# Kernel tuning notes

Hardware: AMD Instinct MI355X
Metric: run time of the kernel (lower is better)

Reference implementation:

```python
import jax, jax.numpy as jnp
import numpy as np

INPUT_SIZE = 84 * 84 * 4  # 28224
FEATURE_SIZE = 1500
BATCH = 256

def setup_inputs() -> dict:
    key = jax.random.key(0)
    k_x, k_we, k_wd = jax.random.split(key, 3)
    scale_e = 1.0 / np.sqrt(INPUT_SIZE)
    scale_d = 1.0 / np.sqrt(FEATURE_SIZE)
    return {
        "x": jax.random.normal(k_x, (BATCH, INPUT_SIZE), dtype=jnp.float32),
        "W_enc": jax.random.normal(k_we, (FEATURE_SIZE, INPUT_SIZE), dtype=jnp.float32) * scale_e,
        "b_enc": jnp.zeros((FEATURE_SIZE,), dtype=jnp.float32),
        "W_dec": jax.random.normal(k_wd, (INPUT_SIZE, FEATURE_SIZE), dtype=jnp.float32) * scale_d,
        "b_dec": jnp.zeros((INPUT_SIZE,), dtype=jnp.float32),
    }

def reference(x, W_enc, b_enc, W_dec, b_dec):
    # Encoder: y_enc = sigmoid(x @ W_enc^T + b_enc), shape [B, F]
    y_enc = jax.nn.sigmoid(jnp.einsum('bi,fi->bf', x, W_enc) + b_enc)
    # Contractive (Jacobian Frobenius norm) term, closed form:
    # d y_enc[b,i] / d x[b,:] = y*(1-y) * W_enc[i,:]
    # jac_reg = sum_{b,i} (y*(1-y))^2 * ||W_enc[i,:]||^2
    s2 = jnp.square(y_enc * (1.0 - y_enc))          # [B, F]
    row_norm2 = jnp.sum(jnp.square(W_enc), axis=1)  # [F]
    jac_reg = jnp.sum(s2 * row_norm2)               # scalar
    # Decoder
    y_out = jax.nn.sigmoid(jnp.einsum('bf,if->bi', y_enc, W_dec) + b_dec)
    return y_out, jac_reg
```

## Files before the change

kernel.cpp:

```cpp
#include <hip/hip_runtime.h>
#include <hip/hip_bf16.h>


#define BATCH 256
#define IN    28224
#define FEAT  1500
#define FPAD  1536
#define LDA   40

typedef __attribute__((ext_vector_type(8))) short short8;
typedef __attribute__((ext_vector_type(4))) float f32x4;

__device__ __forceinline__ unsigned pack2(float lo, float hi) {
    unsigned a = __float_as_uint(lo) + 0x8000u;
    unsigned b = __float_as_uint(hi) + 0x8000u;
    return __builtin_amdgcn_perm(b, a, 0x07060302);
}
__device__ __forceinline__ unsigned short f2bf(float f) {
    unsigned u = __float_as_uint(f);
    return (unsigned short)((u + 0x7FFFu + ((u >> 16) & 1u)) >> 16);
}

__global__ __launch_bounds__(256) void cvt_x(const float* __restrict__ x,
                                             unsigned short* __restrict__ xbf) {
    int idx = blockIdx.x * 256 + threadIdx.x;
    float4 v = ((const float4*)x)[idx];
    ((uint2*)xbf)[idx] = make_uint2(pack2(v.x, v.y), pack2(v.z, v.w));
}

__global__ __launch_bounds__(256) void enc_gemm(const unsigned short* __restrict__ xbf,
                                                const float* __restrict__ We,
                                                float* __restrict__ preact,
                                                float* __restrict__ rn2) {
    __shared__ unsigned short As[256 * LDA];
    __shared__ unsigned short Bs[64 * LDA];

    const int n0 = blockIdx.x * 64;
    const int kb = blockIdx.y * 672;
    const int t    = threadIdx.x;
    const int lane = t & 63;
    const int w    = t >> 6;
    const int l15  = lane & 15;
    const int quad = lane >> 4;

    const unsigned short* asrc = xbf + (long)(t >> 2) * IN + (t & 3) * 8 + kb;
    unsigned short*       adst = As + (t >> 2) * LDA + (t & 3) * 8;
    const int brow = t >> 3;
    const int bc4  = t & 7;
    const int f0 = n0 + brow, f1 = f0 + 32;
    const float* bsrc0 = We + (long)(f0 < FEAT ? f0 : FEAT - 1) * IN + bc4 * 4 + kb;
    const float* bsrc1 = We + (long)(f1 < FEAT ? f1 : FEAT - 1) * IN + bc4 * 4 + kb;
    unsigned short* bdst0 = Bs + brow * LDA + bc4 * 4;
    unsigned short* bdst1 = bdst0 + 32 * LDA;
    float rsq0 = 0.f, rsq1 = 0.f;

    f32x4 acc[4][4];
#pragma unroll
    for (int mt = 0; mt < 4; ++mt)
#pragma unroll
        for (int nt = 0; nt < 4; ++nt) { f32x4 z = {0.f,0.f,0.f,0.f}; acc[mt][nt] = z; }

    for (int k = 0; k < 672; k += 32) {
        short8 av[4];
#pragma unroll
        for (int j = 0; j < 4; ++j)
            av[j] = *(const short8*)(asrc + (long)64 * j * IN + k);
        const float4 bv0 = *(const float4*)(bsrc0 + k);
        const float4 bv1 = *(const float4*)(bsrc1 + k);

        __syncthreads();
#pragma unroll
        for (int j = 0; j < 4; ++j)
            *(short8*)(adst + 64 * j * LDA) = av[j];
        *(uint2*)bdst0 = make_uint2(pack2(bv0.x, bv0.y), pack2(bv0.z, bv0.w));
        *(uint2*)bdst1 = make_uint2(pack2(bv1.x, bv1.y), pack2(bv1.z, bv1.w));
        rsq0 += bv0.x*bv0.x + bv0.y*bv0.y + bv0.z*bv0.z + bv0.w*bv0.w;
        rsq1 += bv1.x*bv1.x + bv1.y*bv1.y + bv1.z*bv1.z + bv1.w*bv1.w;
        __syncthreads();

        short8 a[4], b[4];
#pragma unroll
        for (int mt = 0; mt < 4; ++mt)
            a[mt] = *(const short8*)(As + (w * 64 + mt * 16 + l15) * LDA + quad * 8);
#pragma unroll
        for (int nt = 0; nt < 4; ++nt)
            b[nt] = *(const short8*)(Bs + (nt * 16 + l15) * LDA + quad * 8);
#pragma unroll
        for (int mt = 0; mt < 4; ++mt)
#pragma unroll
            for (int nt = 0; nt < 4; ++nt)
                acc[mt][nt] = __builtin_amdgcn_mfma_f32_16x16x32_bf16(a[mt], b[nt], acc[mt][nt], 0, 0, 0);
    }

#pragma unroll
    for (int nt = 0; nt < 4; ++nt) {
        const int col = n0 + nt * 16 + l15;
        if (col < FEAT) {
#pragma unroll
            for (int mt = 0; mt < 4; ++mt) {
                float* p = preact + (long)(w * 64 + mt * 16 + quad * 4) * FEAT + col;
#pragma unroll
                for (int r = 0; r < 4; ++r) atomicAdd(p + (long)r * FEAT, acc[mt][nt][r]);
            }
        }
    }

    {
        float v0 = rsq0, v1 = rsq1;
#pragma unroll
        for (int off = 1; off < 8; off <<= 1) {
            v0 += __shfl_xor(v0, off);
            v1 += __shfl_xor(v1, off);
        }
        if ((lane & 7) == 0) {
            if (f0 < FEAT) atomicAdd(&rn2[f0], v0);
            if (f1 < FEAT) atomicAdd(&rn2[f1], v1);
        }
    }
}

__global__ __launch_bounds__(256) void act_jac(const float* __restrict__ preact,
                                               const float* __restrict__ be,
                                               const float* __restrict__ rn2,
                                               unsigned short* __restrict__ yenc,
                                               float* __restrict__ jac) {
    const int b = blockIdx.y;
    const int f = blockIdx.x * 256 + threadIdx.x;
    float local = 0.0f;
    unsigned short h = 0;
    if (f < FEAT) {
        float p = preact[b * FEAT + f] + be[f];
        float y = 1.0f / (1.0f + __expf(-p));
        h = f2bf(y);
        float s = y * (1.0f - y);
        local = s * s * rn2[f];
    }
    yenc[b * FPAD + f] = h;

    float v = local;
#pragma unroll
    for (int off = 32; off > 0; off >>= 1) v += __shfl_down(v, off);
    __shared__ float red[4];
    if ((threadIdx.x & 63) == 0) red[threadIdx.x >> 6] = v;
    __syncthreads();
    if (threadIdx.x == 0) atomicAdd(jac, red[0] + red[1] + red[2] + red[3]);
}

__global__ __launch_bounds__(256) void dec_gemm(const unsigned short* __restrict__ yenc,
                                                const float* __restrict__ Wd,
                                                const float* __restrict__ bd,
                                                float* __restrict__ out) {
    __shared__ unsigned short As[128 * LDA];
    __shared__ unsigned short Bs[64 * LDA];

    const int m0 = (blockIdx.x & 1) * 128;
    const int n0 = (blockIdx.x >> 1) * 64;
    const int t    = threadIdx.x;
    const int lane = t & 63;
    const int w    = t >> 6;
    const int l15  = lane & 15;
    const int quad = lane >> 4;
    const int mrow = (w >> 1) * 64;
    const int ncol = (w & 1) * 32;

    const unsigned short* asrc = yenc + (long)(m0 + (t >> 2)) * FPAD + (t & 3) * 8;
    unsigned short*       adst = As + (t >> 2) * LDA + (t & 3) * 8;
    const float* bsrc = Wd + (long)(n0 + (t >> 3)) * FEAT + (t & 7) * 4;
    unsigned short* bdst = Bs + (t >> 3) * LDA + (t & 7) * 4;

    f32x4 acc[4][2];
#pragma unroll
    for (int mt = 0; mt < 4; ++mt)
#pragma unroll
        for (int nt = 0; nt < 2; ++nt) { f32x4 z = {0.f,0.f,0.f,0.f}; acc[mt][nt] = z; }

    for (int k = 0; k < 1504; k += 32) {
        short8 av[2];
#pragma unroll
        for (int j = 0; j < 2; ++j)
            av[j] = *(const short8*)(asrc + (long)64 * j * FPAD + k);
        float4 bv0, bv1;
        if (k < 1472) {
            bv0 = *(const float4*)(bsrc + k);
            bv1 = *(const float4*)(bsrc + (long)32 * FEAT + k);
        } else {
            if ((t & 7) == 7) { bv0 = make_float4(0,0,0,0); bv1 = bv0; }
            else {
                bv0 = *(const float4*)(bsrc + k);
                bv1 = *(const float4*)(bsrc + (long)32 * FEAT + k);
            }
        }

        __syncthreads();
#pragma unroll
        for (int j = 0; j < 2; ++j)
            *(short8*)(adst + 64 * j * LDA) = av[j];
        *(uint2*)bdst              = make_uint2(pack2(bv0.x, bv0.y), pack2(bv0.z, bv0.w));
        *(uint2*)(bdst + 32 * LDA) = make_uint2(pack2(bv1.x, bv1.y), pack2(bv1.z, bv1.w));
        __syncthreads();

        short8 a[4], b[2];
#pragma unroll
        for (int mt = 0; mt < 4; ++mt)
            a[mt] = *(const short8*)(As + (mrow + mt * 16 + l15) * LDA + quad * 8);
#pragma unroll
        for (int nt = 0; nt < 2; ++nt)
            b[nt] = *(const short8*)(Bs + (ncol + nt * 16 + l15) * LDA + quad * 8);
#pragma unroll
        for (int mt = 0; mt < 4; ++mt)
#pragma unroll
            for (int nt = 0; nt < 2; ++nt)
                acc[mt][nt] = __builtin_amdgcn_mfma_f32_16x16x32_bf16(a[mt], b[nt], acc[mt][nt], 0, 0, 0);
    }

#pragma unroll
    for (int nt = 0; nt < 2; ++nt) {
        const int col = n0 + ncol + nt * 16 + l15;
        const float bias = bd[col];
#pragma unroll
        for (int mt = 0; mt < 4; ++mt) {
            const int row = m0 + mrow + mt * 16 + quad * 4;
#pragma unroll
            for (int r = 0; r < 4; ++r) {
                float v = acc[mt][nt][r] + bias;
                out[(long)(row + r) * IN + col] = 1.0f / (1.0f + __expf(-v));
            }
        }
    }
}

extern "C" void kernel_launch(void* const* d_in, const int* in_sizes, int n_in,
                              void* d_out, int out_size, void* d_ws, size_t ws_size,
                              hipStream_t stream) {
    const float* x  = (const float*)d_in[0];
    const float* We = (const float*)d_in[1];
    const float* be = (const float*)d_in[2];
    const float* Wd = (const float*)d_in[3];
    const float* bd = (const float*)d_in[4];
    float* out = (float*)d_out;

    char* ws = (char*)d_ws;
    float* preact        = (float*)ws;
    float* rn2           = (float*)(ws + 1536000);
    unsigned short* yenc = (unsigned short*)(ws + 1542144);
    unsigned short* xbf  = (unsigned short*)(ws + 2328576);

    hipMemsetAsync(ws, 0, 1542144, stream);
    hipMemsetAsync(out + 7225344, 0, 4, stream);

    cvt_x<<<7056, 256, 0, stream>>>(x, xbf);
    enc_gemm<<<dim3(24, 42), 256, 0, stream>>>(xbf, We, preact, rn2);
    act_jac<<<dim3(6, 256), 256, 0, stream>>>(preact, be, rn2, yenc, out + 7225344);
    dec_gemm<<<882, 256, 0, stream>>>(yenc, Wd, bd, out);
}
```

Baseline: 550.9 us.

## Pre-convert weights to bf16 and use async global-to-LDS loads in GEMMs

Adds a path, taken when the workspace is large enough, that converts W_enc and W_dec to bf16 in separate kernels (W_dec padded to a K of 1504) and computes the row norms during conversion. Both GEMMs then load bf16 tiles straight into LDS with global_load_lds. The encoder writes split-K partials to a buffer that the activation kernel sums, replacing the float atomics. This trades an extra full read and write of both weight matrices every call for simpler GEMM inner loops. The old path stays as a fallback for smaller workspaces.

Result: no change. 545.1 us (-1.0%).

```diff
diff --git a/kernel.cpp b/kernel.cpp
--- a/kernel.cpp
+++ b/kernel.cpp
@@ -6,7 +6,8 @@
 #define IN    28224
 #define FEAT  1500
 #define FPAD  1536
-#define LDA   40
+#define KPAD  1504
+#define ENC_S 21
 
 typedef __attribute__((ext_vector_type(8))) short short8;
 typedef __attribute__((ext_vector_type(4))) float f32x4;
@@ -20,6 +21,14 @@
     unsigned u = __float_as_uint(f);
     return (unsigned short)((u + 0x7FFFu + ((u >> 16) & 1u)) >> 16);
 }
+
+__device__ __forceinline__ void async16(const unsigned short* g, unsigned short* l) {
+    __builtin_amdgcn_global_load_lds(
+        (const __attribute__((address_space(1))) unsigned int*)g,
+        (__attribute__((address_space(3))) unsigned int*)l,
+        16, 0, 0);
+}
+
 
 __global__ __launch_bounds__(256) void cvt_x(const float* __restrict__ x,
                                              unsigned short* __restrict__ xbf) {
@@ -27,6 +36,208 @@
     float4 v = ((const float4*)x)[idx];
     ((uint2*)xbf)[idx] = make_uint2(pack2(v.x, v.y), pack2(v.z, v.w));
 }
+
+__global__ __launch_bounds__(256) void wcvt_enc(const float* __restrict__ We,
+                                                unsigned short* __restrict__ Webf,
+                                                float* __restrict__ rn2) {
+    const int row = blockIdx.y;
+    const int t = threadIdx.x;
+    const float4* src = (const float4*)(We + (long)row * IN) + blockIdx.x * 1008;
+    uint2* dst = (uint2*)(Webf + (long)row * IN) + blockIdx.x * 1008;
+    float sq = 0.f;
+#pragma unroll
+    for (int j = 0; j < 4; ++j) {
+        int i = j * 256 + t;
+        if (i < 1008) {
+            float4 v = src[i];
+            dst[i] = make_uint2(pack2(v.x, v.y), pack2(v.z, v.w));
+            sq += v.x*v.x + v.y*v.y + v.z*v.z + v.w*v.w;
+        }
+    }
+#pragma unroll
+    for (int off = 32; off > 0; off >>= 1) sq += __shfl_down(sq, off);
+    __shared__ float red[4];
+    if ((t & 63) == 0) red[t >> 6] = sq;
+    __syncthreads();
+    if (t == 0) atomicAdd(&rn2[row], red[0] + red[1] + red[2] + red[3]);
+}
+
+__global__ __launch_bounds__(256) void wcvt_dec(const float* __restrict__ Wd,
+                                                unsigned short* __restrict__ Wdbf) {
+    int i = blockIdx.x * 256 + threadIdx.x;
+    if (i >= 10584000) return;
+    unsigned row = (unsigned)i / 375u;
+    unsigned c   = (unsigned)i - row * 375u;
+    float4 v = ((const float4*)Wd)[i];
+    uint2* dst = (uint2*)Wdbf + (long)row * 376 + c;
+    *dst = make_uint2(pack2(v.x, v.y), pack2(v.z, v.w));
+    if (c == 374) dst[1] = make_uint2(0u, 0u);
+}
+
+
+__global__ __launch_bounds__(256) void enc_gemm_f(const unsigned short* __restrict__ xbf,
+                                                  const unsigned short* __restrict__ Webf,
+                                                  float* __restrict__ part) {
+    __shared__ unsigned short As[128 * 32];
+    __shared__ unsigned short Bs[64 * 32];
+
+    const int m0 = (blockIdx.x & 1) * 128;
+    const int n0 = (blockIdx.x >> 1) * 64;
+    const int kb = blockIdx.y * 1344;
+    const int t    = threadIdx.x;
+    const int lane = t & 63;
+    const int w    = t >> 6;
+    const int l15  = lane & 15;
+    const int quad = lane >> 4;
+    const int wm   = w & 1;
+    const int wn   = w >> 1;
+
+    const unsigned short* ga0 = xbf + (long)(m0 + w * 32 + (lane >> 2)) * IN + kb + (lane & 3) * 8;
+    const unsigned short* ga1 = ga0 + (long)16 * IN;
+    const unsigned short* gb  = Webf + (long)(n0 + w * 16 + (lane >> 2)) * IN + kb + (lane & 3) * 8;
+    unsigned short* la0 = As + (w * 32) * 32;
+    unsigned short* la1 = As + (w * 32 + 16) * 32;
+    unsigned short* lb  = Bs + (w * 16) * 32;
+
+    f32x4 acc[4][2];
+#pragma unroll
+    for (int mt = 0; mt < 4; ++mt)
+#pragma unroll
+        for (int nt = 0; nt < 2; ++nt) { f32x4 z = {0.f,0.f,0.f,0.f}; acc[mt][nt] = z; }
+
+    for (int k = 0; k < 1344; k += 32) {
+        __syncthreads();
+        async16(ga0 + k, la0);
+        async16(ga1 + k, la1);
+        async16(gb  + k, lb);
+        __syncthreads();
+
+        short8 a[4], b[2];
+#pragma unroll
+        for (int mt = 0; mt < 4; ++mt)
+            a[mt] = *(const short8*)(As + (wm * 64 + mt * 16 + l15) * 32 + quad * 8);
+#pragma unroll
+        for (int nt = 0; nt < 2; ++nt)
+            b[nt] = *(const short8*)(Bs + (wn * 32 + nt * 16 + l15) * 32 + quad * 8);
+#pragma unroll
+        for (int mt = 0; mt < 4; ++mt)
+#pragma unroll
+            for (int nt = 0; nt < 2; ++nt)
+                acc[mt][nt] = __builtin_amdgcn_mfma_f32_16x16x32_bf16(a[mt], b[nt], acc[mt][nt], 0, 0, 0);
+    }
+
+    float* ps = part + (long)blockIdx.y * (BATCH * FPAD);
+#pragma unroll
+    for (int nt = 0; nt < 2; ++nt) {
+        const int col = n0 + wn * 32 + nt * 16 + l15;
+#pragma unroll
+        for (int mt = 0; mt < 4; ++mt) {
+            const int row = m0 + wm * 64 + mt * 16 + quad * 4;
+#pragma unroll
+            for (int r = 0; r < 4; ++r)
+                ps[(long)(row + r) * FPAD + col] = acc[mt][nt][r];
+        }
+    }
+}
+
+__global__ __launch_bounds__(256) void act_jac_f(const float* __restrict__ part,
+                                                 const float* __restrict__ be,
+                                                 const float* __restrict__ rn2,
+                                                 unsigned short* __restrict__ yenc,
+                                                 float* __restrict__ jac) {
+    const int b = blockIdx.y;
+    const int f = blockIdx.x * 256 + threadIdx.x;
+    float local = 0.0f;
+    unsigned short h = 0;
+    if (f < FEAT) {
+        float p = be[f];
+#pragma unroll 3
+        for (int s = 0; s < ENC_S; ++s)
+            p += part[(long)(s * BATCH + b) * FPAD + f];
+        float y = 1.0f / (1.0f + __expf(-p));
+        h = f2bf(y);
+        float sg = y * (1.0f - y);
+        local = sg * sg * rn2[f];
+    }
+    if (f < KPAD) yenc[b * KPAD + f] = h;
+
+    float v = local;
+#pragma unroll
+    for (int off = 32; off > 0; off >>= 1) v += __shfl_down(v, off);
+    __shared__ float red[4];
+    if ((threadIdx.x & 63) == 0) red[threadIdx.x >> 6] = v;
+    __syncthreads();
+    if (threadIdx.x == 0) atomicAdd(jac, red[0] + red[1] + red[2] + red[3]);
+}
+
+__global__ __launch_bounds__(256) void dec_gemm_f(const unsigned short* __restrict__ yenc,
+                                                  const unsigned short* __restrict__ Wdbf,
+                                                  const float* __restrict__ bd,
+                                                  float* __restrict__ out) {
+    __shared__ unsigned short As[128 * 32];
+    __shared__ unsigned short Bs[64 * 32];
+
+    const int m0 = (blockIdx.x & 1) * 128;
+    const int n0 = (blockIdx.x >> 1) * 64;
+    const int t    = threadIdx.x;
+    const int lane = t & 63;
+    const int w    = t >> 6;
+    const int l15  = lane & 15;
+    const int quad = lane >> 4;
+    const int wm   = w & 1;
+    const int wn   = w >> 1;
+
+    const unsigned short* ga0 = yenc + (long)(m0 + w * 32 + (lane >> 2)) * KPAD + (lane & 3) * 8;
+    const unsigned short* ga1 = ga0 + (long)16 * KPAD;
+    const unsigned short* gb  = Wdbf + (long)(n0 + w * 16 + (lane >> 2)) * KPAD + (lane & 3) * 8;
+    unsigned short* la0 = As + (w * 32) * 32;
+    unsigned short* la1 = As + (w * 32 + 16) * 32;
+    unsigned short* lb  = Bs + (w * 16) * 32;
+
+    f32x4 acc[4][2];
+#pragma unroll
+    for (int mt = 0; mt < 4; ++mt)
+#pragma unroll
+        for (int nt = 0; nt < 2; ++nt) { f32x4 z = {0.f,0.f,0.f,0.f}; acc[mt][nt] = z; }
+
+    for (int k = 0; k < KPAD; k += 32) {
+        __syncthreads();
+        async16(ga0 + k, la0);
+        async16(ga1 + k, la1);
+        async16(gb  + k, lb);
+        __syncthreads();
+
+        short8 a[4], b[2];
+#pragma unroll
+        for (int mt = 0; mt < 4; ++mt)
+            a[mt] = *(const short8*)(As + (wm * 64 + mt * 16 + l15) * 32 + quad * 8);
+#pragma unroll
+        for (int nt = 0; nt < 2; ++nt)
+            b[nt] = *(const short8*)(Bs + (wn * 32 + nt * 16 + l15) * 32 + quad * 8);
+#pragma unroll
+        for (int mt = 0; mt < 4; ++mt)
+#pragma unroll
+            for (int nt = 0; nt < 2; ++nt)
+                acc[mt][nt] = __builtin_amdgcn_mfma_f32_16x16x32_bf16(a[mt], b[nt], acc[mt][nt], 0, 0, 0);
+    }
+
+#pragma unroll
+    for (int nt = 0; nt < 2; ++nt) {
+        const int col = n0 + wn * 32 + nt * 16 + l15;
+        const float bias = bd[col];
+#pragma unroll
+        for (int mt = 0; mt < 4; ++mt) {
+            const int row = m0 + wm * 64 + mt * 16 + quad * 4;
+#pragma unroll
+            for (int r = 0; r < 4; ++r) {
+                float v = acc[mt][nt][r] + bias;
+                out[(long)(row + r) * IN + col] = 1.0f / (1.0f + __expf(-v));
+            }
+        }
+    }
+}
+
+#define LDA 40
 
 __global__ __launch_bounds__(256) void enc_gemm(const unsigned short* __restrict__ xbf,
                                                 const float* __restrict__ We,
@@ -34,64 +245,48 @@
                                                 float* __restrict__ rn2) {
     __shared__ unsigned short As[256 * LDA];
     __shared__ unsigned short Bs[64 * LDA];
-
     const int n0 = blockIdx.x * 64;
     const int kb = blockIdx.y * 672;
-    const int t    = threadIdx.x;
-    const int lane = t & 63;
-    const int w    = t >> 6;
-    const int l15  = lane & 15;
-    const int quad = lane >> 4;
-
+    const int t = threadIdx.x, lane = t & 63, w = t >> 6, l15 = lane & 15, quad = lane >> 4;
     const unsigned short* asrc = xbf + (long)(t >> 2) * IN + (t & 3) * 8 + kb;
-    unsigned short*       adst = As + (t >> 2) * LDA + (t & 3) * 8;
-    const int brow = t >> 3;
-    const int bc4  = t & 7;
+    unsigned short* adst = As + (t >> 2) * LDA + (t & 3) * 8;
+    const int brow = t >> 3, bc4 = t & 7;
     const int f0 = n0 + brow, f1 = f0 + 32;
     const float* bsrc0 = We + (long)(f0 < FEAT ? f0 : FEAT - 1) * IN + bc4 * 4 + kb;
     const float* bsrc1 = We + (long)(f1 < FEAT ? f1 : FEAT - 1) * IN + bc4 * 4 + kb;
     unsigned short* bdst0 = Bs + brow * LDA + bc4 * 4;
     unsigned short* bdst1 = bdst0 + 32 * LDA;
     float rsq0 = 0.f, rsq1 = 0.f;
-
     f32x4 acc[4][4];
 #pragma unroll
     for (int mt = 0; mt < 4; ++mt)
 #pragma unroll
         for (int nt = 0; nt < 4; ++nt) { f32x4 z = {0.f,0.f,0.f,0.f}; acc[mt][nt] = z; }
-
     for (int k = 0; k < 672; k += 32) {
         short8 av[4];
 #pragma unroll
-        for (int j = 0; j < 4; ++j)
-            av[j] = *(const short8*)(asrc + (long)64 * j * IN + k);
+        for (int j = 0; j < 4; ++j) av[j] = *(const short8*)(asrc + (long)64 * j * IN + k);
         const float4 bv0 = *(const float4*)(bsrc0 + k);
         const float4 bv1 = *(const float4*)(bsrc1 + k);
-
-        __syncthreads();
-#pragma unroll
-        for (int j = 0; j < 4; ++j)
-            *(short8*)(adst + 64 * j * LDA) = av[j];
+        __syncthreads();
+#pragma unroll
+        for (int j = 0; j < 4; ++j) *(short8*)(adst + 64 * j * LDA) = av[j];
         *(uint2*)bdst0 = make_uint2(pack2(bv0.x, bv0.y), pack2(bv0.z, bv0.w));
         *(uint2*)bdst1 = make_uint2(pack2(bv1.x, bv1.y), pack2(bv1.z, bv1.w));
         rsq0 += bv0.x*bv0.x + bv0.y*bv0.y + bv0.z*bv0.z + bv0.w*bv0.w;
         rsq1 += bv1.x*bv1.x + bv1.y*bv1.y + bv1.z*bv1.z + bv1.w*bv1.w;
         __syncthreads();
-
         short8 a[4], b[4];
 #pragma unroll
-        for (int mt = 0; mt < 4; ++mt)
-            a[mt] = *(const short8*)(As + (w * 64 + mt * 16 + l15) * LDA + quad * 8);
-#pragma unroll
-        for (int nt = 0; nt < 4; ++nt)
-            b[nt] = *(const short8*)(Bs + (nt * 16 + l15) * LDA + quad * 8);
+        for (int mt = 0; mt < 4; ++mt) a[mt] = *(const short8*)(As + (w * 64 + mt * 16 + l15) * LDA + quad * 8);
+#pragma unroll
+        for (int nt = 0; nt < 4; ++nt) b[nt] = *(const short8*)(Bs + (nt * 16 + l15) * LDA + quad * 8);
 #pragma unroll
         for (int mt = 0; mt < 4; ++mt)
 #pragma unroll
             for (int nt = 0; nt < 4; ++nt)
                 acc[mt][nt] = __builtin_amdgcn_mfma_f32_16x16x32_bf16(a[mt], b[nt], acc[mt][nt], 0, 0, 0);
     }
-
 #pragma unroll
     for (int nt = 0; nt < 4; ++nt) {
         const int col = n0 + nt * 16 + l15;
@@ -104,14 +299,10 @@
             }
         }
     }
-
     {
         float v0 = rsq0, v1 = rsq1;
 #pragma unroll
-        for (int off = 1; off < 8; off <<= 1) {
-            v0 += __shfl_xor(v0, off);
-            v1 += __shfl_xor(v1, off);
-        }
+        for (int off = 1; off < 8; off <<= 1) { v0 += __shfl_xor(v0, off); v1 += __shfl_xor(v1, off); }
         if ((lane & 7) == 0) {
             if (f0 < FEAT) atomicAdd(&rn2[f0], v0);
             if (f1 < FEAT) atomicAdd(&rn2[f1], v1);
@@ -136,7 +327,6 @@
         local = s * s * rn2[f];
     }
     yenc[b * FPAD + f] = h;
-
     float v = local;
 #pragma unroll
     for (int off = 32; off > 0; off >>= 1) v += __shfl_down(v, off);
@@ -152,33 +342,23 @@
                                                 float* __restrict__ out) {
     __shared__ unsigned short As[128 * LDA];
     __shared__ unsigned short Bs[64 * LDA];
-
     const int m0 = (blockIdx.x & 1) * 128;
     const int n0 = (blockIdx.x >> 1) * 64;
-    const int t    = threadIdx.x;
-    const int lane = t & 63;
-    const int w    = t >> 6;
-    const int l15  = lane & 15;
-    const int quad = lane >> 4;
-    const int mrow = (w >> 1) * 64;
-    const int ncol = (w & 1) * 32;
-
+    const int t = threadIdx.x, lane = t & 63, w = t >> 6, l15 = lane & 15, quad = lane >> 4;
+    const int mrow = (w >> 1) * 64, ncol = (w & 1) * 32;
     const unsigned short* asrc = yenc + (long)(m0 + (t >> 2)) * FPAD + (t & 3) * 8;
-    unsigned short*       adst = As + (t >> 2) * LDA + (t & 3) * 8;
+    unsigned short* adst = As + (t >> 2) * LDA + (t & 3) * 8;
     const float* bsrc = Wd + (long)(n0 + (t >> 3)) * FEAT + (t & 7) * 4;
     unsigned short* bdst = Bs + (t >> 3) * LDA + (t & 7) * 4;
-
     f32x4 acc[4][2];
 #pragma unroll
     for (int mt = 0; mt < 4; ++mt)
 #pragma unroll
         for (int nt = 0; nt < 2; ++nt) { f32x4 z = {0.f,0.f,0.f,0.f}; acc[mt][nt] = z; }
-
     for (int k = 0; k < 1504; k += 32) {
         short8 av[2];
 #pragma unroll
-        for (int j = 0; j < 2; ++j)
-            av[j] = *(const short8*)(asrc + (long)64 * j * FPAD + k);
+        for (int j = 0; j < 2; ++j) av[j] = *(const short8*)(asrc + (long)64 * j * FPAD + k);
         float4 bv0, bv1;
         if (k < 1472) {
             bv0 = *(const float4*)(bsrc + k);
@@ -190,29 +370,23 @@
                 bv1 = *(const float4*)(bsrc + (long)32 * FEAT + k);
             }
         }
-
-        __syncthreads();
-#pragma unroll
-        for (int j = 0; j < 2; ++j)
-            *(short8*)(adst + 64 * j * LDA) = av[j];
-        *(uint2*)bdst              = make_uint2(pack2(bv0.x, bv0.y), pack2(bv0.z, bv0.w));
+        __syncthreads();
+#pragma unroll
+        for (int j = 0; j < 2; ++j) *(short8*)(adst + 64 * j * LDA) = av[j];
+        *(uint2*)bdst = make_uint2(pack2(bv0.x, bv0.y), pack2(bv0.z, bv0.w));
         *(uint2*)(bdst + 32 * LDA) = make_uint2(pack2(bv1.x, bv1.y), pack2(bv1.z, bv1.w));
         __syncthreads();
-
         short8 a[4], b[2];
 #pragma unroll
-        for (int mt = 0; mt < 4; ++mt)
-            a[mt] = *(const short8*)(As + (mrow + mt * 16 + l15) * LDA + quad * 8);
-#pragma unroll
-        for (int nt = 0; nt < 2; ++nt)
-            b[nt] = *(const short8*)(Bs + (ncol + nt * 16 + l15) * LDA + quad * 8);
+        for (int mt = 0; mt < 4; ++mt) a[mt] = *(const short8*)(As + (mrow + mt * 16 + l15) * LDA + quad * 8);
+#pragma unroll
+        for (int nt = 0; nt < 2; ++nt) b[nt] = *(const short8*)(Bs + (ncol + nt * 16 + l15) * LDA + quad * 8);
 #pragma unroll
         for (int mt = 0; mt < 4; ++mt)
 #pragma unroll
             for (int nt = 0; nt < 2; ++nt)
                 acc[mt][nt] = __builtin_amdgcn_mfma_f32_16x16x32_bf16(a[mt], b[nt], acc[mt][nt], 0, 0, 0);
     }
-
 #pragma unroll
     for (int nt = 0; nt < 2; ++nt) {
         const int col = n0 + ncol + nt * 16 + l15;
@@ -238,18 +412,38 @@
     const float* Wd = (const float*)d_in[3];
     const float* bd = (const float*)d_in[4];
     float* out = (float*)d_out;
-
     char* ws = (char*)d_ws;
-    float* preact        = (float*)ws;
-    float* rn2           = (float*)(ws + 1536000);
-    unsigned short* yenc = (unsigned short*)(ws + 1542144);
-    unsigned short* xbf  = (unsigned short*)(ws + 2328576);
-
-    hipMemsetAsync(ws, 0, 1542144, stream);
-    hipMemsetAsync(out + 7225344, 0, 4, stream);
-
-    cvt_x<<<7056, 256, 0, stream>>>(x, xbf);
-    enc_gemm<<<dim3(24, 42), 256, 0, stream>>>(xbf, We, preact, rn2);
-    act_jac<<<dim3(6, 256), 256, 0, stream>>>(preact, be, rn2, yenc, out + 7225344);
-    dec_gemm<<<882, 256, 0, stream>>>(yenc, Wd, bd, out);
-}
+
+    if (ws_size >= 219858944ull) {
+        unsigned short* Webf = (unsigned short*)ws;
+        unsigned short* Wdbf = (unsigned short*)(ws + 86704128);
+        unsigned short* xbf  = (unsigned short*)(ws + 171601920);
+        unsigned short* yenc = (unsigned short*)(ws + 186052608);
+        float* part          = (float*)(ws + 186822656);
+        float* rn2           = (float*)(ws + 219852800);
+
+        hipMemsetAsync(ws + 84672000, 0, 2032128, stream);
+        hipMemsetAsync(rn2, 0, 6144, stream);
+        hipMemsetAsync(out + 7225344, 0, 4, stream);
+
+        cvt_x<<<7056, 256, 0, stream>>>(x, xbf);
+        wcvt_enc<<<dim3(7, 1500), 256, 0, stream>>>(We, Webf, rn2);
+        wcvt_dec<<<41344, 256, 0, stream>>>(Wd, Wdbf);
+        enc_gemm_f<<<dim3(48, ENC_S), 256, 0, stream>>>(xbf, Webf, part);
+        act_jac_f<<<dim3(6, 256), 256, 0, stream>>>(part, be, rn2, yenc, out + 7225344);
+        dec_gemm_f<<<882, 256, 0, stream>>>(yenc, Wdbf, bd, out);
+    } else {
+        float* preact        = (float*)ws;
+        float* rn2           = (float*)(ws + 1536000);
+        unsigned short* yenc = (unsigned short*)(ws + 1542144);
+        unsigned short* xbf  = (unsigned short*)(ws + 2328576);
+
+        hipMemsetAsync(ws, 0, 1542144, stream);
+        hipMemsetAsync(out + 7225344, 0, 4, stream);
+
+        cvt_x<<<7056, 256, 0, stream>>>(x, xbf);
+        enc_gemm<<<dim3(24, 42), 256, 0, stream>>>(xbf, We, preact, rn2);
+        act_jac<<<dim3(6, 256), 256, 0, stream>>>(preact, be, rn2, yenc, out + 7225344);
+        dec_gemm<<<882, 256, 0, stream>>>(yenc, Wd, bd, out);
+    }
+}
```
